# Performance work log

Measured on AMD Instinct MI355X. Metric: run time of the kernel, lower is better.

Reference implementation:

```python
import jax, jax.numpy as jnp
import numpy as np

S, B, E, H, V = 256, 64, 256, 512, 32000
PAD_ID = 0


def setup_inputs() -> dict:
    key = jax.random.key(0)
    ks = jax.random.split(key, 12)
    sc = 0.05
    return {
        "sentences": jax.random.randint(ks[0], (S, B), 0, V, dtype=jnp.int64),
        "noise": jax.random.uniform(ks[1], (S, B), dtype=jnp.float32),
        "emb_table": jax.random.normal(ks[2], (V, E), dtype=jnp.float32) * sc,
        "Wih_f": jax.random.normal(ks[3], (3 * H, E), dtype=jnp.float32) * sc,
        "Whh_f": jax.random.normal(ks[4], (3 * H, H), dtype=jnp.float32) * sc,
        "bih_f": jnp.zeros((3 * H,), dtype=jnp.float32),
        "bhh_f": jnp.zeros((3 * H,), dtype=jnp.float32),
        "Wih_b": jax.random.normal(ks[5], (3 * H, E), dtype=jnp.float32) * sc,
        "Whh_b": jax.random.normal(ks[6], (3 * H, H), dtype=jnp.float32) * sc,
        "bih_b": jnp.zeros((3 * H,), dtype=jnp.float32),
        "bhh_b": jnp.zeros((3 * H,), dtype=jnp.float32),
        "zW": jax.random.normal(ks[7], (2 * H,), dtype=jnp.float32) * sc,
        "zb": jnp.zeros((), dtype=jnp.float32),
    }


def _gru_scan(xs, h0, Wih, Whh, bih, bhh):
    # xs: [S,B,E], h0: [B,H]; torch GRU gate order: r, z, n
    def step(h, x):
        gi = x @ Wih.T + bih            # [B,3H]
        gh = h @ Whh.T + bhh            # [B,3H]
        i_r, i_z, i_n = jnp.split(gi, 3, axis=-1)
        h_r, h_z, h_n = jnp.split(gh, 3, axis=-1)
        r = jax.nn.sigmoid(i_r + h_r)
        zg = jax.nn.sigmoid(i_z + h_z)
        n = jnp.tanh(i_n + r * h_n)
        h_new = (1.0 - zg) * n + zg * h
        return h_new, h_new
    _, hs = jax.lax.scan(step, h0, xs)
    return hs                           # [S,B,H]


def reference(sentences, noise, emb_table, Wih_f, Whh_f, bih_f, bhh_f,
              Wih_b, Whh_b, bih_b, bhh_b, zW, zb):
    emb = emb_table[sentences]                       # [S,B,E]
    h0 = jnp.zeros((B, H), dtype=emb.dtype)
    hs_f = _gru_scan(emb, h0, Wih_f, Whh_f, bih_f, bhh_f)
    hs_b = _gru_scan(emb[::-1], h0, Wih_b, Whh_b, bih_b, bhh_b)[::-1]
    hidden = jnp.concatenate([hs_f, hs_b], axis=-1)  # [S,B,2H]
    pz = jax.nn.sigmoid(jnp.einsum('sbh,h->sb', hidden, zW) + zb)  # [S,B]
    # Bernoulli sample (deterministic via supplied uniform noise)
    z = (noise < pz).astype(pz.dtype)                # [S,B]
    z_sizes = z.sum(axis=0).astype(jnp.int32)        # [B]
    # Ragged compaction: selected tokens moved to the front of each column,
    # padded with pad_id (replaces the per-sample masked_select loop).
    mask = z > 0.5
    order = jnp.argsort(jnp.where(mask, 0, 1), axis=0, stable=True)  # [S,B]
    gathered = jnp.take_along_axis(sentences, order, axis=0)         # [S,B]
    pos = jnp.arange(S, dtype=jnp.int32)[:, None]
    rationales = jnp.where(pos < z_sizes[None, :], gathered, PAD_ID)
    return (pz, z, rationales, z_sizes)
```

## Files before the change

### kernel.cpp

```cpp
#include <hip/hip_runtime.h>
#include <math.h>

#define S_LEN 256
#define BATCH 64
#define EDIM  256
#define HDIM  512

typedef float f32x4 __attribute__((ext_vector_type(4)));

__device__ __forceinline__ void ld_b128_sc(f32x4* v, const float* p) {
  asm volatile("global_load_dwordx4 %0, %1, off sc0 sc1"
               : "=v"(*v) : "v"(p) : "memory");
}
__device__ __forceinline__ void st_b128_sc(float* p, f32x4 v) {
  asm volatile("global_store_dwordx4 %0, %1, off sc0 sc1"
               :: "v"(p), "v"(v) : "memory");
}

__global__ __launch_bounds__(512) void gi_gemm(
    const int* __restrict__ sent, const float* __restrict__ emb,
    const float* __restrict__ Wih_f, const float* __restrict__ bih_f,
    const float* __restrict__ Wih_b, const float* __restrict__ bih_b,
    float* __restrict__ gi, int abs_base, int buf_base, int dstride)
{
  const int d  = blockIdx.z;
  const int bx = blockIdx.x;
  const int by = blockIdx.y;
  const float* W    = d ? Wih_b : Wih_f;
  const float* bias = d ? bih_b : bih_f;

  __shared__ int    tok[128];
  __shared__ float4 As4[128][8];
  __shared__ float4 Bs4[128][8];

  const int tid = threadIdx.x;
  if (tid < 128) {
    int s_lc = 2 * bx + (tid >> 6);
    int slot = abs_base + s_lc;
    int srow = (d == 0) ? slot : (S_LEN - 1 - slot);
    tok[tid] = sent[srow * BATCH + (tid & 63)];
  }

  float acc[8][4];
#pragma unroll
  for (int i = 0; i < 8; ++i)
#pragma unroll
    for (int j = 0; j < 4; ++j) acc[i][j] = 0.f;

  const int tb = tid & 15;
  const int tn = tid >> 4;

  for (int kc = 0; kc < 8; ++kc) {
    __syncthreads();
#pragma unroll
    for (int it = 0; it < 2; ++it) {
      int flat = tid + 512 * it;
      int row  = flat >> 3;
      int k4   = flat & 7;
      int sw   = k4 ^ (row & 7) ^ ((row >> 3) & 7);
      As4[row][sw] = *(const float4*)&emb[(size_t)tok[row] * EDIM + kc * 32 + 4 * k4];
      Bs4[row][sw] = *(const float4*)&W[(size_t)(by * 128 + row) * EDIM + kc * 32 + 4 * k4];
    }
    __syncthreads();
#pragma unroll
    for (int k4 = 0; k4 < 8; ++k4) {
      float4 a[8];
#pragma unroll
      for (int i = 0; i < 8; ++i)
        a[i] = As4[8 * tb + i][k4 ^ i ^ (tb & 7)];
#pragma unroll
      for (int j = 0; j < 4; ++j) {
        int r = 4 * tn + j;
        float4 bf = Bs4[r][k4 ^ (r & 7) ^ ((r >> 3) & 7)];
#pragma unroll
        for (int i = 0; i < 8; ++i)
          acc[i][j] += a[i].x * bf.x + a[i].y * bf.y
                     + a[i].z * bf.z + a[i].w * bf.w;
      }
    }
  }

  const int s_lc = 2 * bx + (tb >> 3);
  const int brow = 8 * (tb & 7);
#pragma unroll
  for (int j = 0; j < 4; ++j) {
    int n = by * 128 + 4 * tn + j;
    float bs = bias[n];
    int g = n >> 9, u = n & 511;
    size_t base = ((((size_t)d * dstride + buf_base + s_lc) * 3 + g) * HDIM + u) * BATCH + brow;
    float4 v0 = { acc[0][j] + bs, acc[1][j] + bs, acc[2][j] + bs, acc[3][j] + bs };
    float4 v1 = { acc[4][j] + bs, acc[5][j] + bs, acc[6][j] + bs, acc[7][j] + bs };
    *(float4*)&gi[base]     = v0;
    *(float4*)&gi[base + 4] = v1;
  }
}

#define GBUF ((size_t)2 * 64 * 3 * HDIM * BATCH)

__global__ __launch_bounds__(256, 1) void mega_kernel(
    const int* __restrict__ sent, const float* __restrict__ emb,
    const float* __restrict__ Wih_f, const float* __restrict__ bih_f,
    const float* __restrict__ Wih_b, const float* __restrict__ bih_b,
    float* __restrict__ gi, float* __restrict__ hs,
    const float* __restrict__ Whh_f, const float* __restrict__ bhh_f,
    const float* __restrict__ Whh_b, const float* __restrict__ bhh_b,
    unsigned* cnt)
{
  const int w   = blockIdx.x;
  const int d   = w >> 7;
  const int ub  = w & 127;
  const int tid = threadIdx.x;
  const int tx  = tid & 63;
  const int ty  = __builtin_amdgcn_readfirstlane(tid >> 6);
  const int u   = 4 * ub + ty;

  const float* Whh = d ? Whh_b : Whh_f;
  const float* bhh = d ? bhh_b : bhh_f;
  const float* Wih = d ? Wih_b : Wih_f;
  const float* bih = d ? bih_b : bih_f;

  __shared__ float whl[12][512];
  __shared__ float wihl[12][256];
  __shared__ float hl[64][260];
  __shared__ float hb[64][4];

#pragma unroll
  for (int it = 0; it < 6; ++it) {
    int flat = tid + 256 * it;
    int wrow = flat >> 7;
    int c4   = flat & 127;
    int tyw  = wrow / 3, g = wrow % 3;
    *(f32x4*)&whl[wrow][4 * c4] =
        *(const f32x4*)&Whh[(size_t)(g * HDIM + 4 * ub + tyw) * HDIM + 4 * c4];
  }
#pragma unroll
  for (int it = 0; it < 3; ++it) {
    int flat = tid + 256 * it;
    int wrow = flat >> 6;
    int c4   = flat & 63;
    int tyw  = wrow / 3, g = wrow % 3;
    *(f32x4*)&wihl[wrow][4 * c4] =
        *(const f32x4*)&Wih[(size_t)(g * HDIM + 4 * ub + tyw) * EDIM + 4 * c4];
  }
  __syncthreads();

  const float br = bhh[u];
  const float bz = bhh[512 + u];
  const float bn = bhh[1024 + u];
  const float bir = bih[u], biz = bih[512 + u], bin = bih[1024 + u];
  const float* wR = &whl[ty * 3 + 0][0];
  const float* wZ = &whl[ty * 3 + 1][0];
  const float* wN = &whl[ty * 3 + 2][0];
  const float* iR = &wihl[ty * 3 + 0][0];
  const float* iZ = &wihl[ty * 3 + 1][0];
  const float* iN = &wihl[ty * 3 + 2][0];
  const int uhalf = u >> 8, ulo = u & 255;
  const int arr_line = (16 * d + (w & 15)) << 4;

#define GBP(s) (gi + (size_t)(((s) >> 6) & 1) * GBUF \
                   + ((size_t)(d * 64 + ((s) & 63)) * 3) * (HDIM * BATCH))

  float ir, iz, in_;
  {
    const float* gb = GBP(0);
    ir  = gb[((size_t)0 * HDIM + u) * BATCH + tx];
    iz  = gb[((size_t)1 * HDIM + u) * BATCH + tx];
    in_ = gb[((size_t)2 * HDIM + u) * BATCH + tx];
  }

  for (int gs = 0; gs < S_LEN; ++gs) {
    const int t_store = (d == 0) ? gs : (S_LEN - 1 - gs);
    const int t_prev  = (d == 0) ? (gs - 1) : (S_LEN - gs);

    float aR = 0.f, aZ = 0.f, aN = 0.f, hp = 0.f;

    if (gs > 0) {
      const float* hpg = hs + ((size_t)d * S_LEN + t_prev) * HDIM * BATCH;
      f32x4 buf[32];
#pragma unroll
      for (int j = 0; j < 32; ++j) {
        int half = j >> 4;
        int flat = tid + 256 * (j & 15);
        ld_b128_sc(&buf[j], &hpg[(size_t)(flat >> 6) * HDIM + half * 256 + 4 * (flat & 63)]);
      }
      asm volatile("s_waitcnt vmcnt(16)" ::: "memory");
      __builtin_amdgcn_sched_barrier(0);
#pragma unroll
      for (int j = 0; j < 16; ++j) {
        int flat = tid + 256 * j;
        *(f32x4*)&hl[flat >> 6][4 * (flat & 63)] = buf[j];
      }
      __syncthreads();

      if (uhalf == 0) hp = hl[tx][ulo];
      {
        const float* hrow = &hl[tx][0];
#pragma unroll 4
        for (int kk = 0; kk < 256; kk += 4) {
          f32x4 h4  = *(const f32x4*)&hrow[kk];
          f32x4 w4r = *(const f32x4*)&wR[kk];
          f32x4 w4z = *(const f32x4*)&wZ[kk];
          f32x4 w4n = *(const f32x4*)&wN[kk];
          aR += h4.x * w4r.x + h4.y * w4r.y + h4.z * w4r.z + h4.w * w4r.w;
          aZ += h4.x * w4z.x + h4.y * w4z.y + h4.z * w4z.z + h4.w * w4z.w;
          aN += h4.x * w4n.x + h4.y * w4n.y + h4.z * w4n.z + h4.w * w4n.w;
        }
      }
      __syncthreads();
      asm volatile("s_waitcnt vmcnt(0)" ::: "memory");
      __builtin_amdgcn_sched_barrier(0);
#pragma unroll
      for (int j = 16; j < 32; ++j) {
        int flat = tid + 256 * (j & 15);
        *(f32x4*)&hl[flat >> 6][4 * (flat & 63)] = buf[j];
      }
      __syncthreads();

      if (uhalf == 1) hp = hl[tx][ulo];
      {
        const float* hrow = &hl[tx][0];
#pragma unroll 4
        for (int kk = 0; kk < 256; kk += 4) {
          f32x4 h4  = *(const f32x4*)&hrow[kk];
          f32x4 w4r = *(const f32x4*)&wR[256 + kk];
          f32x4 w4z = *(const f32x4*)&wZ[256 + kk];
          f32x4 w4n = *(const f32x4*)&wN[256 + kk];
          aR += h4.x * w4r.x + h4.y * w4r.y + h4.z * w4r.z + h4.w * w4r.w;
          aZ += h4.x * w4z.x + h4.y * w4z.y + h4.z * w4z.z + h4.w * w4z.w;
          aN += h4.x * w4n.x + h4.y * w4n.y + h4.z * w4n.z + h4.w * w4n.w;
        }
      }
    }

    float r  = 1.f / (1.f + expf(-(ir + aR + br)));
    float zg = 1.f / (1.f + expf(-(iz + aZ + bz)));
    float n  = tanhf(in_ + r * (aN + bn));
    float hn = (1.f - zg) * n + zg * hp;

    __syncthreads();
    hb[tx][ty] = hn;
    __syncthreads();
    if (tid < 64) {
      f32x4 v = *(const f32x4*)&hb[tid][0];
      st_b128_sc(&hs[(((size_t)d * S_LEN + t_store) * BATCH + tid) * HDIM + 4 * ub], v);
      asm volatile("s_waitcnt vmcnt(0)" ::: "memory");
    }
    if (tid == 0)
      __hip_atomic_fetch_add(&cnt[arr_line], 1u,
                             __ATOMIC_RELAXED, __HIP_MEMORY_SCOPE_AGENT);

    if (gs + 1 < S_LEN) {
      const float* gb = GBP(gs + 1);
      ir  = gb[((size_t)0 * HDIM + u) * BATCH + tx];
      iz  = gb[((size_t)1 * HDIM + u) * BATCH + tx];
      in_ = gb[((size_t)2 * HDIM + u) * BATCH + tx];
    }

    if (gs + 64 < S_LEN) {
      const int sp   = gs + 64;
      const int srow = (d == 0) ? sp : (S_LEN - 1 - sp);
      const int tk   = sent[srow * BATCH + tx];
      const float* ep = emb + (size_t)tk * EDIM;
      float g0 = 0.f, g1 = 0.f, g2 = 0.f;
#pragma unroll 8
      for (int m = 0; m < 64; ++m) {
        f32x4 e  = *(const f32x4*)&ep[4 * m];
        f32x4 wa = *(const f32x4*)&iR[4 * m];
        f32x4 wb = *(const f32x4*)&iZ[4 * m];
        f32x4 wc = *(const f32x4*)&iN[4 * m];
        g0 += e.x * wa.x + e.y * wa.y + e.z * wa.z + e.w * wa.w;
        g1 += e.x * wb.x + e.y * wb.y + e.z * wb.z + e.w * wb.w;
        g2 += e.x * wc.x + e.y * wc.y + e.z * wc.z + e.w * wc.w;
      }
      float* gw = GBP(sp);
      gw[((size_t)0 * HDIM + u) * BATCH + tx] = g0 + bir;
      gw[((size_t)1 * HDIM + u) * BATCH + tx] = g1 + biz;
      gw[((size_t)2 * HDIM + u) * BATCH + tx] = g2 + bin;
    }

    if (tid < 16) {
      unsigned tgt = 8u * (unsigned)(gs + 1);
      while (__hip_atomic_load(&cnt[(16 * d + tid) << 4],
                               __ATOMIC_RELAXED, __HIP_MEMORY_SCOPE_AGENT) < tgt)
        __builtin_amdgcn_s_sleep(1);
    }
    __syncthreads();
  }
#undef GBP
}

__global__ __launch_bounds__(256, 1) void scan_kernel(
    const float* __restrict__ gi, float* __restrict__ hs,
    const float* __restrict__ Whh_f, const float* __restrict__ bhh_f,
    const float* __restrict__ Whh_b, const float* __restrict__ bhh_b,
    unsigned* cnt, int step0, int nsteps)
{
  const int w   = blockIdx.x;
  const int d   = w >> 7;
  const int ub  = w & 127;
  const int tid = threadIdx.x;
  const int tx  = tid & 63;
  const int ty  = __builtin_amdgcn_readfirstlane(tid >> 6);
  const int u   = 4 * ub + ty;

  const float* Whh = d ? Whh_b : Whh_f;
  const float* bhh = d ? bhh_b : bhh_f;

  __shared__ float whl[12][512];
  __shared__ float hl2[2][64][260];
  __shared__ float hb[64][4];

#pragma unroll
  for (int it = 0; it < 6; ++it) {
    int flat = tid + 256 * it;
    int wrow = flat >> 7;
    int c4   = flat & 127;
    int tyw  = wrow / 3, g = wrow % 3;
    *(f32x4*)&whl[wrow][4 * c4] =
        *(const f32x4*)&Whh[(size_t)(g * HDIM + 4 * ub + tyw) * HDIM + 4 * c4];
  }
  __syncthreads();

  const float br = bhh[u];
  const float bz = bhh[512 + u];
  const float bn = bhh[1024 + u];
  const float* wR = &whl[ty * 3 + 0][0];
  const float* wZ = &whl[ty * 3 + 1][0];
  const float* wN = &whl[ty * 3 + 2][0];
  const int uhalf = u >> 8, ulo = u & 255;
  const int arr_line = (16 * d + (w & 15)) << 4;

  float ir, iz, in_;
  {
    const float* gb = gi + ((size_t)d * nsteps) * 3 * HDIM * BATCH;
    ir  = gb[((size_t)0 * HDIM + u) * BATCH + tx];
    iz  = gb[((size_t)1 * HDIM + u) * BATCH + tx];
    in_ = gb[((size_t)2 * HDIM + u) * BATCH + tx];
  }

  for (int l = 0; l < nsteps; ++l) {
    const int gs      = step0 + l;
    const int t_store = (d == 0) ? gs : (S_LEN - 1 - gs);
    const int t_prev  = (d == 0) ? (gs - 1) : (S_LEN - gs);

    float aR = 0.f, aZ = 0.f, aN = 0.f, hp = 0.f;

    if (gs > 0) {
      const float* hpg = hs + ((size_t)d * S_LEN + t_prev) * HDIM * BATCH;
      f32x4 buf[32];
#pragma unroll
      for (int j = 0; j < 32; ++j) {
        int half = j >> 4;
        int flat = tid + 256 * (j & 15);
        ld_b128_sc(&buf[j], &hpg[(size_t)(flat >> 6) * HDIM + half * 256 + 4 * (flat & 63)]);
      }
      asm volatile("s_waitcnt vmcnt(16)" ::: "memory");
      __builtin_amdgcn_sched_barrier(0);
#pragma unroll
      for (int j = 0; j < 16; ++j) {
        int flat = tid + 256 * j;
        *(f32x4*)&hl2[0][flat >> 6][4 * (flat & 63)] = buf[j];
      }
      __syncthreads();

      if (uhalf == 0) hp = hl2[0][tx][ulo];
      {
        const float* hrow = &hl2[0][tx][0];
#pragma unroll 4
        for (int kk = 0; kk < 256; kk += 4) {
          f32x4 h4  = *(const f32x4*)&hrow[kk];
          f32x4 w4r = *(const f32x4*)&wR[kk];
          f32x4 w4z = *(const f32x4*)&wZ[kk];
          f32x4 w4n = *(const f32x4*)&wN[kk];
          aR += h4.x * w4r.x + h4.y * w4r.y + h4.z * w4r.z + h4.w * w4r.w;
          aZ += h4.x * w4z.x + h4.y * w4z.y + h4.z * w4z.z + h4.w * w4z.w;
          aN += h4.x * w4n.x + h4.y * w4n.y + h4.z * w4n.z + h4.w * w4n.w;
        }
      }

      asm volatile("s_waitcnt vmcnt(0)" ::: "memory");
      __builtin_amdgcn_sched_barrier(0);
#pragma unroll
      for (int j = 16; j < 32; ++j) {
        int flat = tid + 256 * (j & 15);
        *(f32x4*)&hl2[1][flat >> 6][4 * (flat & 63)] = buf[j];
      }
      __syncthreads();

      if (uhalf == 1) hp = hl2[1][tx][ulo];
      {
        const float* hrow = &hl2[1][tx][0];
#pragma unroll 4
        for (int kk = 0; kk < 256; kk += 4) {
          f32x4 h4  = *(const f32x4*)&hrow[kk];
          f32x4 w4r = *(const f32x4*)&wR[256 + kk];
          f32x4 w4z = *(const f32x4*)&wZ[256 + kk];
          f32x4 w4n = *(const f32x4*)&wN[256 + kk];
          aR += h4.x * w4r.x + h4.y * w4r.y + h4.z * w4r.z + h4.w * w4r.w;
          aZ += h4.x * w4z.x + h4.y * w4z.y + h4.z * w4z.z + h4.w * w4z.w;
          aN += h4.x * w4n.x + h4.y * w4n.y + h4.z * w4n.z + h4.w * w4n.w;
        }
      }
    }

    float r  = 1.f / (1.f + expf(-(ir + aR + br)));
    float zg = 1.f / (1.f + expf(-(iz + aZ + bz)));
    float n  = tanhf(in_ + r * (aN + bn));
    float hn = (1.f - zg) * n + zg * hp;

    __syncthreads();
    hb[tx][ty] = hn;
    __syncthreads();
    if (tid < 64) {
      f32x4 v = *(const f32x4*)&hb[tid][0];
      st_b128_sc(&hs[(((size_t)d * S_LEN + t_store) * BATCH + tid) * HDIM + 4 * ub], v);
      asm volatile("s_waitcnt vmcnt(0)" ::: "memory");
    }
    if (tid == 0)
      __hip_atomic_fetch_add(&cnt[arr_line], 1u,
                             __ATOMIC_RELAXED, __HIP_MEMORY_SCOPE_AGENT);
    if (l + 1 < nsteps) {
      const float* gb = gi + ((size_t)d * nsteps + l + 1) * 3 * HDIM * BATCH;
      ir  = gb[((size_t)0 * HDIM + u) * BATCH + tx];
      iz  = gb[((size_t)1 * HDIM + u) * BATCH + tx];
      in_ = gb[((size_t)2 * HDIM + u) * BATCH + tx];
    }
    if (tid < 16) {
      unsigned tgt = 8u * (unsigned)(gs + 1);
      while (__hip_atomic_load(&cnt[(16 * d + tid) << 4],
                               __ATOMIC_RELAXED, __HIP_MEMORY_SCOPE_AGENT) < tgt)
        __builtin_amdgcn_s_sleep(1);
    }
    __syncthreads();
  }
}

__global__ __launch_bounds__(256) void pz_kernel(
    const float* __restrict__ hs, const float* __restrict__ zW,
    const float* __restrict__ zb_, const float* __restrict__ noise,
    float* __restrict__ out)
{
  const int gtid = blockIdx.x * 256 + threadIdx.x;
  const int wave = gtid >> 6;
  const int lane = threadIdx.x & 63;
  const float zb = zb_[0];
  float4 w1 = *(const float4*)&zW[lane * 8];
  float4 w2 = *(const float4*)&zW[lane * 8 + 4];
  float4 w3 = *(const float4*)&zW[512 + lane * 8];
  float4 w4 = *(const float4*)&zW[512 + lane * 8 + 4];
  for (int r = wave; r < S_LEN * BATCH; r += 1024) {
    const float* hf  = hs + (size_t)r * HDIM;
    const float* hbk = hs + (size_t)(S_LEN * BATCH + r) * HDIM;
    float4 a1 = *(const float4*)&hf[lane * 8];
    float4 a2 = *(const float4*)&hf[lane * 8 + 4];
    float4 b1 = *(const float4*)&hbk[lane * 8];
    float4 b2 = *(const float4*)&hbk[lane * 8 + 4];
    float acc = a1.x * w1.x + a1.y * w1.y + a1.z * w1.z + a1.w * w1.w
              + a2.x * w2.x + a2.y * w2.y + a2.z * w2.z + a2.w * w2.w
              + b1.x * w3.x + b1.y * w3.y + b1.z * w3.z + b1.w * w3.w
              + b2.x * w4.x + b2.y * w4.y + b2.z * w4.z + b2.w * w4.w;
#pragma unroll
    for (int off = 32; off > 0; off >>= 1) acc += __shfl_down(acc, off, 64);
    if (lane == 0) {
      float p = 1.f / (1.f + expf(-(acc + zb)));
      out[r] = p;
      out[S_LEN * BATCH + r] = (noise[r] < p) ? 1.f : 0.f;
    }
  }
}

__global__ __launch_bounds__(256) void rat_kernel(
    const int* __restrict__ sent, float* __restrict__ out)
{
  const int b = blockIdx.x;
  const int s = threadIdx.x;
  __shared__ int ps[256];
  const int z = (out[S_LEN * BATCH + s * BATCH + b] > 0.5f) ? 1 : 0;
  ps[s] = z;
  __syncthreads();
#pragma unroll
  for (int off = 1; off < 256; off <<= 1) {
    int v = (s >= off) ? ps[s - off] : 0;
    __syncthreads();
    ps[s] += v;
    __syncthreads();
  }
  const int incl  = ps[s];
  const int total = ps[255];
  const int pos   = incl - z;
  if (z) out[2 * S_LEN * BATCH + pos * BATCH + b] = (float)sent[s * BATCH + b];
  if (s >= total) out[2 * S_LEN * BATCH + s * BATCH + b] = 0.f;
  if (s == 0) out[3 * S_LEN * BATCH + b] = (float)total;
}

extern "C" void kernel_launch(void* const* d_in, const int* in_sizes, int n_in,
                              void* d_out, int out_size, void* d_ws, size_t ws_size,
                              hipStream_t stream)
{
  const int*   sent  = (const int*)  d_in[0];
  const float* noise = (const float*)d_in[1];
  const float* emb   = (const float*)d_in[2];
  const float* Wih_f = (const float*)d_in[3];
  const float* Whh_f = (const float*)d_in[4];
  const float* bih_f = (const float*)d_in[5];
  const float* bhh_f = (const float*)d_in[6];
  const float* Wih_b = (const float*)d_in[7];
  const float* Whh_b = (const float*)d_in[8];
  const float* bih_b = (const float*)d_in[9];
  const float* bhh_b = (const float*)d_in[10];
  const float* zW    = (const float*)d_in[11];
  const float* zb    = (const float*)d_in[12];
  float* out = (float*)d_out;

  float* base = (float*)d_ws;
  unsigned* cnt = (unsigned*)base;
  float* hs = base + 1024;
  float* gi = hs + (size_t)2 * S_LEN * HDIM * BATCH;

  const size_t HS_BYTES = (size_t)2 * S_LEN * HDIM * BATCH * 4;
  const size_t NEED_MEGA = 4096 + HS_BYTES + 2 * GBUF * 4;

  (void)hipMemsetAsync(cnt, 0, 4096, stream);
  if (ws_size >= NEED_MEGA) {
    gi_gemm<<<dim3(32, 12, 2), 512, 0, stream>>>(
        sent, emb, Wih_f, bih_f, Wih_b, bih_b, gi, 0, 0, 64);
    mega_kernel<<<dim3(256), 256, 0, stream>>>(
        sent, emb, Wih_f, bih_f, Wih_b, bih_b, gi, hs,
        Whh_f, bhh_f, Whh_b, bhh_b, cnt);
  } else {
    for (int c = 0; c < 4; ++c) {
      gi_gemm<<<dim3(32, 12, 2), 512, 0, stream>>>(
          sent, emb, Wih_f, bih_f, Wih_b, bih_b, gi, 64 * c, 0, 64);
      scan_kernel<<<dim3(256), 256, 0, stream>>>(
          gi, hs, Whh_f, bhh_f, Whh_b, bhh_b, cnt, 64 * c, 64);
    }
  }
  pz_kernel<<<dim3(256), 256, 0, stream>>>(hs, zW, zb, noise, out);
  rat_kernel<<<dim3(BATCH), 256, 0, stream>>>(sent, out);
}
```

Baseline: 4.884 ms.

## Compute input-gate projections inline per step instead of via gi buffer

Removes the upfront gi_gemm launch and the global gi ring buffer. Each block now computes its input-gate projections for the next timestep inline, after signalling completion and before waiting at the barrier. This saves a kernel launch, the prologue GEMM and the global memory traffic for gi, and it also lowers the workspace requirement. In exchange the per-step embedding dot products now sit on the serial recurrence loop rather than being prefetched 64 steps ahead, so their latency may not be fully hidden by the barrier wait.

```diff
diff --git a/kernel.cpp b/kernel.cpp
--- a/kernel.cpp
+++ b/kernel.cpp
@@ -101,7 +101,7 @@
     const int* __restrict__ sent, const float* __restrict__ emb,
     const float* __restrict__ Wih_f, const float* __restrict__ bih_f,
     const float* __restrict__ Wih_b, const float* __restrict__ bih_b,
-    float* __restrict__ gi, float* __restrict__ hs,
+    float* __restrict__ hs,
     const float* __restrict__ Whh_f, const float* __restrict__ bhh_f,
     const float* __restrict__ Whh_b, const float* __restrict__ bhh_b,
     unsigned* cnt)
@@ -157,16 +157,27 @@
   const int uhalf = u >> 8, ulo = u & 255;
   const int arr_line = (16 * d + (w & 15)) << 4;
 
-#define GBP(s) (gi + (size_t)(((s) >> 6) & 1) * GBUF \
-                   + ((size_t)(d * 64 + ((s) & 63)) * 3) * (HDIM * BATCH))
-
   float ir, iz, in_;
-  {
-    const float* gb = GBP(0);
-    ir  = gb[((size_t)0 * HDIM + u) * BATCH + tx];
-    iz  = gb[((size_t)1 * HDIM + u) * BATCH + tx];
-    in_ = gb[((size_t)2 * HDIM + u) * BATCH + tx];
-  }
+#define INLINE_GI(S)                                                        \
+  {                                                                         \
+    const int srow = (d == 0) ? (S) : (S_LEN - 1 - (S));                    \
+    const int tk   = sent[srow * BATCH + tx];                               \
+    const float* ep = emb + (size_t)tk * EDIM;                              \
+    float g0 = 0.f, g1 = 0.f, g2 = 0.f;                                     \
+    _Pragma("unroll 8")                                                     \
+    for (int m = 0; m < 64; ++m) {                                          \
+      f32x4 e  = *(const f32x4*)&ep[4 * m];                                 \
+      f32x4 wa = *(const f32x4*)&iR[4 * m];                                 \
+      f32x4 wb = *(const f32x4*)&iZ[4 * m];                                 \
+      f32x4 wc = *(const f32x4*)&iN[4 * m];                                 \
+      g0 += e.x * wa.x + e.y * wa.y + e.z * wa.z + e.w * wa.w;              \
+      g1 += e.x * wb.x + e.y * wb.y + e.z * wb.z + e.w * wb.w;              \
+      g2 += e.x * wc.x + e.y * wc.y + e.z * wc.z + e.w * wc.w;              \
+    }                                                                       \
+    ir = g0 + bir; iz = g1 + biz; in_ = g2 + bin;                           \
+  }
+
+  INLINE_GI(0)
 
   for (int gs = 0; gs < S_LEN; ++gs) {
     const int t_store = (d == 0) ? gs : (S_LEN - 1 - gs);
@@ -249,34 +260,7 @@
       __hip_atomic_fetch_add(&cnt[arr_line], 1u,
                              __ATOMIC_RELAXED, __HIP_MEMORY_SCOPE_AGENT);
 
-    if (gs + 1 < S_LEN) {
-      const float* gb = GBP(gs + 1);
-      ir  = gb[((size_t)0 * HDIM + u) * BATCH + tx];
-      iz  = gb[((size_t)1 * HDIM + u) * BATCH + tx];
-      in_ = gb[((size_t)2 * HDIM + u) * BATCH + tx];
-    }
-
-    if (gs + 64 < S_LEN) {
-      const int sp   = gs + 64;
-      const int srow = (d == 0) ? sp : (S_LEN - 1 - sp);
-      const int tk   = sent[srow * BATCH + tx];
-      const float* ep = emb + (size_t)tk * EDIM;
-      float g0 = 0.f, g1 = 0.f, g2 = 0.f;
-#pragma unroll 8
-      for (int m = 0; m < 64; ++m) {
-        f32x4 e  = *(const f32x4*)&ep[4 * m];
-        f32x4 wa = *(const f32x4*)&iR[4 * m];
-        f32x4 wb = *(const f32x4*)&iZ[4 * m];
-        f32x4 wc = *(const f32x4*)&iN[4 * m];
-        g0 += e.x * wa.x + e.y * wa.y + e.z * wa.z + e.w * wa.w;
-        g1 += e.x * wb.x + e.y * wb.y + e.z * wb.z + e.w * wb.w;
-        g2 += e.x * wc.x + e.y * wc.y + e.z * wc.z + e.w * wc.w;
-      }
-      float* gw = GBP(sp);
-      gw[((size_t)0 * HDIM + u) * BATCH + tx] = g0 + bir;
-      gw[((size_t)1 * HDIM + u) * BATCH + tx] = g1 + biz;
-      gw[((size_t)2 * HDIM + u) * BATCH + tx] = g2 + bin;
-    }
+    if (gs + 1 < S_LEN) INLINE_GI(gs + 1)
 
     if (tid < 16) {
       unsigned tgt = 8u * (unsigned)(gs + 1);
@@ -286,7 +270,7 @@
     }
     __syncthreads();
   }
-#undef GBP
+#undef INLINE_GI
 }
 
 __global__ __launch_bounds__(256, 1) void scan_kernel(
@@ -518,14 +502,11 @@
   float* gi = hs + (size_t)2 * S_LEN * HDIM * BATCH;
 
   const size_t HS_BYTES = (size_t)2 * S_LEN * HDIM * BATCH * 4;
-  const size_t NEED_MEGA = 4096 + HS_BYTES + 2 * GBUF * 4;
 
   (void)hipMemsetAsync(cnt, 0, 4096, stream);
-  if (ws_size >= NEED_MEGA) {
-    gi_gemm<<<dim3(32, 12, 2), 512, 0, stream>>>(
-        sent, emb, Wih_f, bih_f, Wih_b, bih_b, gi, 0, 0, 64);
+  if (ws_size >= 4096 + HS_BYTES) {
     mega_kernel<<<dim3(256), 256, 0, stream>>>(
-        sent, emb, Wih_f, bih_f, Wih_b, bih_b, gi, hs,
+        sent, emb, Wih_f, bih_f, Wih_b, bih_b, hs,
         Whh_f, bhh_f, Whh_b, bhh_b, cnt);
   } else {
     for (int c = 0; c < 4; ++c) {
```

Measured after the change: 4.605 ms. 5.7% less time.
